# Optimization experiments

Measured on AMD Instinct MI355X. Metric: run time of the kernel, lower is better.

## Reference

```python
import jax, jax.numpy as jnp
import numpy as np

NUM_HEADS = 8
NUM_GROUPS = 32  # min(C//4, 32) for C=512
EPS = 1e-6       # flax GroupNorm default


def setup_inputs() -> dict:
    key = jax.random.key(0)
    ks = jax.random.split(key, 3)
    B, H, W, D, C = 2, 16, 16, 16, 512
    x = jax.random.normal(ks[0], (B, H, W, D, C), dtype=jnp.float32)
    w_qkv = jax.random.normal(ks[1], (C, 3 * C), dtype=jnp.float32) / np.sqrt(C)
    w_proj = jax.random.normal(ks[2], (C, C), dtype=jnp.float32) / np.sqrt(C)
    return {
        "x": x,
        "gn_scale": jnp.ones((C,), jnp.float32),
        "gn_bias": jnp.zeros((C,), jnp.float32),
        "w_qkv": w_qkv,
        "b_qkv": jnp.zeros((3 * C,), jnp.float32),
        "w_proj": w_proj,
        "b_proj": jnp.zeros((C,), jnp.float32),
    }


def group_norm(x, scale, bias):
    # x: [B, S, C]; normalize within each of NUM_GROUPS channel groups over (S, group-channels)
    B, S, C = x.shape
    xg = x.reshape(B, S, NUM_GROUPS, C // NUM_GROUPS)
    mean = jnp.mean(xg, axis=(1, 3), keepdims=True)
    var = jnp.var(xg, axis=(1, 3), keepdims=True)
    xn = (xg - mean) * jax.lax.rsqrt(var + EPS)
    return xn.reshape(B, S, C) * scale + bias


def reference(x, gn_scale, gn_bias, w_qkv, b_qkv, w_proj, b_proj):
    B, H, W, D, C = x.shape
    S = H * W * D
    hd = C // NUM_HEADS
    xf = x.reshape(B, S, C)
    q_in = group_norm(xf, gn_scale, gn_bias)
    # 1x1x1 conv == per-position dense
    qkv = q_in @ w_qkv + b_qkv                      # [B, S, 3C]
    qkv = qkv.reshape(B, S, NUM_HEADS, 3 * hd)
    q, k, v = jnp.split(qkv, 3, axis=-1)            # each [B, S, nh, hd]
    scale = 1.0 / jnp.sqrt(jnp.asarray(hd, x.dtype))
    logits = jnp.einsum('btnh,bfnh->bnft', k, q * scale)  # [B, nh, S, S]
    weights = jax.nn.softmax(logits, axis=-1)
    h = jnp.einsum('bnft,btnh->bfnh', weights, v)   # [B, S, nh, hd]
    h = h.reshape(B, S, C) @ w_proj + b_proj
    return h.reshape(x.shape) + x
```

## Files before the change

### kernel.cpp

```cpp
#include <hip/hip_runtime.h>

typedef __attribute__((ext_vector_type(8))) short short8;
typedef __attribute__((ext_vector_type(4))) float f32x4;
typedef __attribute__((ext_vector_type(16))) float f32x16;

#define S_LEN 4096
#define C_DIM 512
#define NH 8
#define HD 64
#define NG 32
#define GS 16
#define LOG2E 1.44269504088896340736f

__device__ __forceinline__ unsigned short f2bf(float f) {
  union { float f; unsigned int u; } v; v.f = f;
  unsigned int r = v.u + 0x7fffu + ((v.u >> 16) & 1u);
  return (unsigned short)(r >> 16);
}

__device__ __forceinline__ float fexp2(float x) {
  float r;
  asm("v_exp_f32 %0, %1" : "=v"(r) : "v"(x));
  return r;
}

__device__ __forceinline__ unsigned pk_bf16(float a, float b) {
  unsigned r;
  asm("v_cvt_pk_bf16_f32 %0, %1, %2" : "=v"(r) : "v"(a), "v"(b));
  return r;
}

__device__ __forceinline__ void pl_swap(unsigned& a, unsigned& b) {
  asm("v_permlane32_swap_b32 %0, %1" : "+v"(a), "+v"(b));
}

__device__ __forceinline__ void gload_lds16(const void* g, void* l) {
  __builtin_amdgcn_global_load_lds((const __attribute__((address_space(1))) void*)g,
                                   (__attribute__((address_space(3))) void*)l, 16, 0, 0);
}

__global__ __launch_bounds__(256) void prep_kernel(const float* __restrict__ x,
                                                   float* __restrict__ partials,
                                                   const float* __restrict__ w_qkv,
                                                   unsigned short* __restrict__ wqkvT,
                                                   const float* __restrict__ w_proj,
                                                   unsigned short* __restrict__ wprojT) {
  __shared__ float tile[32][33];
  __shared__ float r1[4], r2[4];
  int bid = blockIdx.x;
  if (bid < 256) {
    int bg = bid >> 2, chunk = bid & 3;
    int b = bg >> 5, g = bg & 31;
    const float* xp = x + (size_t)b * S_LEN * C_DIM + g * GS;
    float s1 = 0.f, s2 = 0.f;
    for (int i = threadIdx.x; i < 1024 * 4; i += 256) {
      int s = chunk * 1024 + (i >> 2), c4 = i & 3;
      float4 v = *(const float4*)&xp[(size_t)s * C_DIM + c4 * 4];
      s1 += v.x + v.y + v.z + v.w;
      s2 += v.x * v.x + v.y * v.y + v.z * v.z + v.w * v.w;
    }
    for (int off = 1; off < 64; off <<= 1) {
      s1 += __shfl_xor(s1, off);
      s2 += __shfl_xor(s2, off);
    }
    int w = threadIdx.x >> 6;
    if ((threadIdx.x & 63) == 0) { r1[w] = s1; r2[w] = s2; }
    __syncthreads();
    if (threadIdx.x == 0) {
      partials[bg * 8 + chunk * 2]     = r1[0] + r1[1] + r1[2] + r1[3];
      partials[bg * 8 + chunk * 2 + 1] = r2[0] + r2[1] + r2[2] + r2[3];
    }
    return;
  }
  const float* src; unsigned short* dst; int K, N, n0, k0;
  if (bid < 1024) {
    int t = bid - 256;  src = w_qkv;  dst = wqkvT;  K = 512; N = 1536;
    n0 = (t % 48) * 32; k0 = (t / 48) * 32;
  } else {
    int t = bid - 1024; src = w_proj; dst = wprojT; K = 512; N = 512;
    n0 = (t % 16) * 32; k0 = (t / 16) * 32;
  }
  int c = threadIdx.x & 31, r0 = threadIdx.x >> 5;
  for (int i = 0; i < 4; ++i) {
    int r = r0 + i * 8;
    tile[r][c] = src[(size_t)(k0 + r) * N + n0 + c];
  }
  __syncthreads();
  for (int i = 0; i < 4; ++i) {
    int r = r0 + i * 8;
    dst[(size_t)(n0 + r) * K + k0 + c] = f2bf(tile[c][r]);
  }
}

__global__ __launch_bounds__(256) void gn_apply_kernel(const float* __restrict__ x,
                                                       const float* __restrict__ partials,
                                                       const float* __restrict__ scale,
                                                       const float* __restrict__ bias,
                                                       unsigned short* __restrict__ out) {
  int idx = blockIdx.x * 256 + threadIdx.x;
  int e = idx * 4;
  int c = e & (C_DIM - 1);
  int bs = e >> 9;
  int b = bs >> 12;
  int grp = b * NG + (c >> 4);
  float s1 = partials[grp * 8] + partials[grp * 8 + 2] + partials[grp * 8 + 4] + partials[grp * 8 + 6];
  float s2 = partials[grp * 8 + 1] + partials[grp * 8 + 3] + partials[grp * 8 + 5] + partials[grp * 8 + 7];
  const float invN = 1.0f / (float)(S_LEN * GS);
  float mean = s1 * invN;
  float var = s2 * invN - mean * mean;
  float rstd = rsqrtf(var + 1e-6f);
  float4 v = *(const float4*)&x[e];
  ushort4 o;
  o.x = f2bf((v.x - mean) * rstd * scale[c]     + bias[c]);
  o.y = f2bf((v.y - mean) * rstd * scale[c + 1] + bias[c + 1]);
  o.z = f2bf((v.z - mean) * rstd * scale[c + 2] + bias[c + 2]);
  o.w = f2bf((v.w - mean) * rstd * scale[c + 3] + bias[c + 3]);
  *(ushort4*)&out[e] = o;
}

template <int MODE>
__global__ __launch_bounds__(256) void gemm_kernel(const unsigned short* __restrict__ A,
                                                   const unsigned short* __restrict__ Bt,
                                                   const float* __restrict__ bias,
                                                   unsigned short* __restrict__ qh,
                                                   unsigned short* __restrict__ kh,
                                                   unsigned short* __restrict__ vh,
                                                   const float* __restrict__ resid,
                                                   float* __restrict__ outf,
                                                   int K) {
  __shared__ unsigned short Alds[128][72];
  __shared__ unsigned short Blds[128][72];
  int tid = threadIdx.x, lane = tid & 63, w = tid >> 6;
  int li = lane & 15, g = lane >> 4;
  int wr = (w >> 1) * 64, wc = (w & 1) * 64;
  int m0 = blockIdx.y * 128, n0 = blockIdx.x * 128;
  f32x4 acc[4][4];
  for (int i = 0; i < 4; ++i)
    for (int j = 0; j < 4; ++j) acc[i][j] = (f32x4){0.f, 0.f, 0.f, 0.f};

  for (int k0 = 0; k0 < K; k0 += 64) {
    for (int i = 0; i < 4; ++i) {
      int ch = tid + i * 256;
      int r = ch >> 3, c8 = (ch & 7) * 8;
      *(int4*)&Alds[r][c8] = *(const int4*)&A[(size_t)(m0 + r) * K + k0 + c8];
      *(int4*)&Blds[r][c8] = *(const int4*)&Bt[(size_t)(n0 + r) * K + k0 + c8];
    }
    __syncthreads();
    for (int ks = 0; ks < 2; ++ks) {
      short8 af[4], bfm[4];
      for (int mi = 0; mi < 4; ++mi)
        af[mi] = *(const short8*)&Alds[wr + mi * 16 + li][ks * 32 + g * 8];
      for (int ni = 0; ni < 4; ++ni)
        bfm[ni] = *(const short8*)&Blds[wc + ni * 16 + li][ks * 32 + g * 8];
      for (int mi = 0; mi < 4; ++mi)
        for (int ni = 0; ni < 4; ++ni)
          acc[mi][ni] = __builtin_amdgcn_mfma_f32_16x16x32_bf16(af[mi], bfm[ni], acc[mi][ni], 0, 0, 0);
    }
    __syncthreads();
  }

  if (MODE == 0) {
    for (int ni = 0; ni < 4; ++ni) {
      int n = n0 + wc + ni * 16 + li;
      float bn = bias[n];
      int head = n / 192;
      int rem = n - head * 192;
      int part = rem >> 6;
      int h = rem & 63;
      unsigned short* dst = part == 0 ? qh : (part == 1 ? kh : vh);
      float mul = part == 0 ? 0.125f * LOG2E : 1.0f;
      for (int mi = 0; mi < 4; ++mi)
        for (int j = 0; j < 4; ++j) {
          int m = m0 + wr + mi * 16 + g * 4 + j;
          int b = m >> 12, s = m & 4095;
          float val = (acc[mi][ni][j] + bn) * mul;
          size_t idx;
          if (part == 2) idx = ((size_t)(b * NH + head) * HD + h) * S_LEN + s;
          else           idx = ((size_t)(b * NH + head) * S_LEN + s) * HD + h;
          dst[idx] = f2bf(val);
        }
    }
  } else {
    for (int ni = 0; ni < 4; ++ni) {
      int n = n0 + wc + ni * 16 + li;
      float bn = bias[n];
      for (int mi = 0; mi < 4; ++mi)
        for (int j = 0; j < 4; ++j) {
          int m = m0 + wr + mi * 16 + g * 4 + j;
          size_t off = (size_t)m * C_DIM + n;
          outf[off] = acc[mi][ni][j] + bn + resid[off];
        }
    }
  }
}

template <int SPLIT>
__global__ __launch_bounds__(256, 4) void attn_kernel(const unsigned short* __restrict__ qh,
                                                      const unsigned short* __restrict__ kh,
                                                      const unsigned short* __restrict__ vt,
                                                      unsigned short* __restrict__ ob,
                                                      float* __restrict__ part) {
  __shared__ unsigned char Kt[2][4096];
  __shared__ unsigned char Vt[2][4096];
  int bn = blockIdx.y;
  int half = SPLIT == 2 ? blockIdx.z : 0;
  int tid = threadIdx.x, lane = tid & 63, wv = tid >> 6;
  int r32 = lane & 31, hi = lane >> 5;
  int q0 = blockIdx.x * 128 + wv * 32;
  const int NT = S_LEN / 32 / SPLIT;
  const unsigned short* qp = qh + (size_t)bn * S_LEN * HD;
  const char* kp = (const char*)(kh + (size_t)bn * S_LEN * HD);
  const char* vp = (const char*)(vt + (size_t)bn * HD * S_LEN);

  int srow  = wv * 8 + (lane >> 3);
  int scolS = (lane & 7) * 16;
  int sc    = scolS ^ ((srow & 7) << 4);
  const char* kSrc = kp + (size_t)srow * 128 + sc + (size_t)half * (S_LEN / 2) * 128;
  int vh_ = srow + ((sc >> 6) << 5);
  const char* vSrc = vp + (size_t)vh_ * (S_LEN * 2) + (sc & 63) + (size_t)half * (S_LEN / 2) * 2;

  short8 qf[4];
#pragma unroll
  for (int ks = 0; ks < 4; ++ks)
    qf[ks] = *(const short8*)&qp[(size_t)(q0 + r32) * HD + ks * 16 + hi * 8];

  union { unsigned u[4]; short8 v; } ones;
#pragma unroll
  for (int i = 0; i < 4; ++i) ones.u[i] = 0x3F803F80u;

  f32x16 o0, o1, lacc;
#pragma unroll
  for (int i = 0; i < 16; ++i) { o0[i] = 0.f; o1[i] = 0.f; lacc[i] = 0.f; }

  int swzr = (r32 & 7) << 4;
  const unsigned char* Kr0 = &Kt[0][r32 * 128];
  const unsigned char* Vr0 = &Vt[0][r32 * 128];

  gload_lds16(kSrc, &Kt[0][wv * 1024]);
  gload_lds16(vSrc, &Vt[0][wv * 1024]);
  __syncthreads();

  for (int it = 0; it < NT; ++it) {
    int buf = it & 1;
    if (it < NT - 1) {
      size_t t0n = (size_t)(it + 1) * 32;
      gload_lds16(kSrc + t0n * 128, &Kt[buf ^ 1][wv * 1024]);
      gload_lds16(vSrc + t0n * 2,   &Vt[buf ^ 1][wv * 1024]);
    }

    const unsigned char* Kr = Kr0 + buf * 4096;
    const unsigned char* Vr = Vr0 + buf * 4096;
    short8 kf[4], vf[4];
#pragma unroll
    for (int ks = 0; ks < 4; ++ks)
      kf[ks] = *(const short8*)&Kr[(ks * 32 + hi * 16) ^ swzr];
#pragma unroll
    for (int kk = 0; kk < 2; ++kk)
#pragma unroll
      for (int hf = 0; hf < 2; ++hf)
        vf[kk * 2 + hf] = *(const short8*)&Vr[(hf * 64 + kk * 32 + hi * 16) ^ swzr];

    f32x16 s;
#pragma unroll
    for (int i = 0; i < 16; ++i) s[i] = 0.f;
#pragma unroll
    for (int ks = 0; ks < 4; ++ks)
      s = __builtin_amdgcn_mfma_f32_32x32x16_bf16(kf[ks], qf[ks], s, 0, 0, 0);

#pragma unroll
    for (int i = 0; i < 16; ++i) s[i] = fexp2(s[i]);

    unsigned pkv[8];
#pragma unroll
    for (int g2 = 0; g2 < 8; ++g2) pkv[g2] = pk_bf16(s[2 * g2], s[2 * g2 + 1]);
    pl_swap(pkv[0], pkv[2]); pl_swap(pkv[1], pkv[3]);
    pl_swap(pkv[4], pkv[6]); pl_swap(pkv[5], pkv[7]);
    union { unsigned u[4]; short8 v; } F0, F1;
    F0.u[0] = pkv[0]; F0.u[1] = pkv[1]; F0.u[2] = pkv[2]; F0.u[3] = pkv[3];
    F1.u[0] = pkv[4]; F1.u[1] = pkv[5]; F1.u[2] = pkv[6]; F1.u[3] = pkv[7];

    o0 = __builtin_amdgcn_mfma_f32_32x32x16_bf16(vf[0], F0.v, o0, 0, 0, 0);
    o1 = __builtin_amdgcn_mfma_f32_32x32x16_bf16(vf[1], F0.v, o1, 0, 0, 0);
    lacc = __builtin_amdgcn_mfma_f32_32x32x16_bf16(ones.v, F0.v, lacc, 0, 0, 0);
    o0 = __builtin_amdgcn_mfma_f32_32x32x16_bf16(vf[2], F1.v, o0, 0, 0, 0);
    o1 = __builtin_amdgcn_mfma_f32_32x32x16_bf16(vf[3], F1.v, o1, 0, 0, 0);
    lacc = __builtin_amdgcn_mfma_f32_32x32x16_bf16(ones.v, F1.v, lacc, 0, 0, 0);

    __syncthreads();
  }

  if (SPLIT == 1) {
    float inv = 1.0f / lacc[0];
    int b = bn >> 3, n = bn & 7;
    size_t base = ((size_t)(b * S_LEN + q0 + r32)) * C_DIM + n * HD;
#pragma unroll
    for (int r = 0; r < 16; ++r) {
      int hrow = (r & 3) + 8 * (r >> 2) + 4 * hi;
      ob[base + hrow]      = f2bf(o0[r] * inv);
      ob[base + 32 + hrow] = f2bf(o1[r] * inv);
    }
  } else {
    float* pp = part + (((size_t)(bn * 2 + half) * S_LEN) + q0 + r32) * 68;
#pragma unroll
    for (int r = 0; r < 16; ++r) {
      int hrow = (r & 3) + 8 * (r >> 2) + 4 * hi;
      pp[hrow]      = o0[r];
      pp[32 + hrow] = o1[r];
    }
    if (!hi) pp[64] = lacc[0];
  }
}

__global__ __launch_bounds__(256) void attn_combine_kernel(const float* __restrict__ part,
                                                           unsigned short* __restrict__ ob) {
  int idx = blockIdx.x * 256 + threadIdx.x;
  int h0 = (idx & 7) * 8;
  int q  = (idx >> 3) & (S_LEN - 1);
  int bn = idx >> 15;
  const float* pA = part + (((size_t)(bn * 2 + 0) * S_LEN) + q) * 68;
  const float* pB = part + (((size_t)(bn * 2 + 1) * S_LEN) + q) * 68;
  float inv = 1.0f / (pA[64] + pB[64]);
  float4 a0 = *(const float4*)&pA[h0], a1 = *(const float4*)&pA[h0 + 4];
  float4 b0 = *(const float4*)&pB[h0], b1 = *(const float4*)&pB[h0 + 4];
  union { unsigned short us[8]; short8 v; } R;
  R.us[0] = f2bf((a0.x + b0.x) * inv); R.us[1] = f2bf((a0.y + b0.y) * inv);
  R.us[2] = f2bf((a0.z + b0.z) * inv); R.us[3] = f2bf((a0.w + b0.w) * inv);
  R.us[4] = f2bf((a1.x + b1.x) * inv); R.us[5] = f2bf((a1.y + b1.y) * inv);
  R.us[6] = f2bf((a1.z + b1.z) * inv); R.us[7] = f2bf((a1.w + b1.w) * inv);
  int b = bn >> 3, n = bn & 7;
  *(short8*)&ob[((size_t)(b * S_LEN + q)) * C_DIM + n * HD + h0] = R.v;
}

extern "C" void kernel_launch(void* const* d_in, const int* in_sizes, int n_in,
                              void* d_out, int out_size, void* d_ws, size_t ws_size,
                              hipStream_t stream) {
  const float* x        = (const float*)d_in[0];
  const float* gn_scale = (const float*)d_in[1];
  const float* gn_bias  = (const float*)d_in[2];
  const float* w_qkv    = (const float*)d_in[3];
  const float* b_qkv    = (const float*)d_in[4];
  const float* w_proj   = (const float*)d_in[5];
  const float* b_proj   = (const float*)d_in[6];
  float* out = (float*)d_out;

  char* ws = (char*)d_ws;
  unsigned short* q_in   = (unsigned short*)(ws);
  unsigned short* wqkvT  = (unsigned short*)(ws + 8388608);
  unsigned short* wprojT = (unsigned short*)(ws + 9961472);
  unsigned short* qhb    = (unsigned short*)(ws + 10485760);
  unsigned short* khb    = (unsigned short*)(ws + 18874368);
  unsigned short* vtb    = (unsigned short*)(ws + 27262976);
  unsigned short* ahb    = (unsigned short*)(ws + 35651584);
  float* partials        = (float*)(ws + 44040192);
  float* opart           = (float*)(ws + 44042240);
  const size_t WS_NEED_SPLIT = 44042240ull + (size_t)16 * 2 * S_LEN * 68 * 4;

  prep_kernel<<<1280, 256, 0, stream>>>(x, partials, w_qkv, wqkvT, w_proj, wprojT);
  gn_apply_kernel<<<4096, 256, 0, stream>>>(x, partials, gn_scale, gn_bias, q_in);
  gemm_kernel<0><<<dim3(12, 64), 256, 0, stream>>>(q_in, wqkvT, b_qkv, qhb, khb, vtb, nullptr, nullptr, 512);
  if (ws_size >= WS_NEED_SPLIT) {
    attn_kernel<2><<<dim3(32, 16, 2), 256, 0, stream>>>(qhb, khb, vtb, ahb, opart);
    attn_combine_kernel<<<2048, 256, 0, stream>>>(opart, ahb);
  } else {
    attn_kernel<1><<<dim3(32, 16, 1), 256, 0, stream>>>(qhb, khb, vtb, ahb, nullptr);
  }
  gemm_kernel<1><<<dim3(4, 64), 256, 0, stream>>>(ahb, wprojT, b_proj, nullptr, nullptr, nullptr, x, out, 512);
}
```

Before: 162.3 us.

## Triple-buffer attention K/V tiles and store split partials in bf16

The attention loop now uses three LDS buffers for K and V, prefetching two tiles ahead. Each iteration waits with an explicit vmcnt(2) wait plus a raw barrier instead of a full __syncthreads, so global loads overlap more with the MFMA work. The split-K partial outputs are stored as packed bf16 with a float row sum, which halves partial-buffer traffic in both the attention and combine kernels. The first QK MFMA also starts from a zero register instead of a zeroed accumulator. In exchange, LDS use grows, which can reduce occupancy, and the partials lose precision before the combine step.

```diff
diff --git a/kernel.cpp b/kernel.cpp
--- a/kernel.cpp
+++ b/kernel.cpp
@@ -199,9 +199,9 @@
                                                       const unsigned short* __restrict__ kh,
                                                       const unsigned short* __restrict__ vt,
                                                       unsigned short* __restrict__ ob,
-                                                      float* __restrict__ part) {
-  __shared__ unsigned char Kt[2][4096];
-  __shared__ unsigned char Vt[2][4096];
+                                                      unsigned short* __restrict__ part) {
+  __shared__ unsigned char Kt[3 * 4096];
+  __shared__ unsigned char Vt[3 * 4096];
   int bn = blockIdx.y;
   int half = SPLIT == 2 ? blockIdx.z : 0;
   int tid = threadIdx.x, lane = tid & 63, wv = tid >> 6;
@@ -228,28 +228,31 @@
 #pragma unroll
   for (int i = 0; i < 4; ++i) ones.u[i] = 0x3F803F80u;
 
-  f32x16 o0, o1, lacc;
-#pragma unroll
-  for (int i = 0; i < 16; ++i) { o0[i] = 0.f; o1[i] = 0.f; lacc[i] = 0.f; }
+  f32x16 o0, o1, lacc, z16;
+#pragma unroll
+  for (int i = 0; i < 16; ++i) { o0[i] = 0.f; o1[i] = 0.f; lacc[i] = 0.f; z16[i] = 0.f; }
 
   int swzr = (r32 & 7) << 4;
-  const unsigned char* Kr0 = &Kt[0][r32 * 128];
-  const unsigned char* Vr0 = &Vt[0][r32 * 128];
-
-  gload_lds16(kSrc, &Kt[0][wv * 1024]);
-  gload_lds16(vSrc, &Vt[0][wv * 1024]);
-  __syncthreads();
-
+  int sBase = wv * 1024;
+
+  gload_lds16(kSrc, &Kt[sBase]);
+  gload_lds16(vSrc, &Vt[sBase]);
+  gload_lds16(kSrc + 32 * 128, &Kt[4096 + sBase]);
+  gload_lds16(vSrc + 32 * 2,   &Vt[4096 + sBase]);
+  asm volatile("s_waitcnt vmcnt(2)" ::: "memory");
+  __builtin_amdgcn_s_barrier();
+
+  int curO = 0, nxtO = 4096, nnO = 8192;
   for (int it = 0; it < NT; ++it) {
-    int buf = it & 1;
-    if (it < NT - 1) {
-      size_t t0n = (size_t)(it + 1) * 32;
-      gload_lds16(kSrc + t0n * 128, &Kt[buf ^ 1][wv * 1024]);
-      gload_lds16(vSrc + t0n * 2,   &Vt[buf ^ 1][wv * 1024]);
-    }
-
-    const unsigned char* Kr = Kr0 + buf * 4096;
-    const unsigned char* Vr = Vr0 + buf * 4096;
+    bool more = (it + 2 < NT);
+    if (more) {
+      size_t t0n = (size_t)(it + 2) * 32;
+      gload_lds16(kSrc + t0n * 128, &Kt[nnO + sBase]);
+      gload_lds16(vSrc + t0n * 2,   &Vt[nnO + sBase]);
+    }
+
+    const unsigned char* Kr = &Kt[curO + r32 * 128];
+    const unsigned char* Vr = &Vt[curO + r32 * 128];
     short8 kf[4], vf[4];
 #pragma unroll
     for (int ks = 0; ks < 4; ++ks)
@@ -260,11 +263,9 @@
       for (int hf = 0; hf < 2; ++hf)
         vf[kk * 2 + hf] = *(const short8*)&Vr[(hf * 64 + kk * 32 + hi * 16) ^ swzr];
 
-    f32x16 s;
-#pragma unroll
-    for (int i = 0; i < 16; ++i) s[i] = 0.f;
-#pragma unroll
-    for (int ks = 0; ks < 4; ++ks)
+    f32x16 s = __builtin_amdgcn_mfma_f32_32x32x16_bf16(kf[0], qf[0], z16, 0, 0, 0);
+#pragma unroll
+    for (int ks = 1; ks < 4; ++ks)
       s = __builtin_amdgcn_mfma_f32_32x32x16_bf16(kf[ks], qf[ks], s, 0, 0, 0);
 
 #pragma unroll
@@ -286,7 +287,10 @@
     o1 = __builtin_amdgcn_mfma_f32_32x32x16_bf16(vf[3], F1.v, o1, 0, 0, 0);
     lacc = __builtin_amdgcn_mfma_f32_32x32x16_bf16(ones.v, F1.v, lacc, 0, 0, 0);
 
-    __syncthreads();
+    if (more) asm volatile("s_waitcnt vmcnt(2)" ::: "memory");
+    else      asm volatile("s_waitcnt vmcnt(0)" ::: "memory");
+    __builtin_amdgcn_s_barrier();
+    int t = curO; curO = nxtO; nxtO = nnO; nnO = t;
   }
 
   if (SPLIT == 1) {
@@ -300,35 +304,39 @@
       ob[base + 32 + hrow] = f2bf(o1[r] * inv);
     }
   } else {
-    float* pp = part + (((size_t)(bn * 2 + half) * S_LEN) + q0 + r32) * 68;
-#pragma unroll
-    for (int r = 0; r < 16; ++r) {
+    unsigned short* pp = part + (((size_t)(bn * 2 + half) * S_LEN) + q0 + r32) * 72;
+#pragma unroll
+    for (int i = 0; i < 8; ++i) {
+      int r = 2 * i;
       int hrow = (r & 3) + 8 * (r >> 2) + 4 * hi;
-      pp[hrow]      = o0[r];
-      pp[32 + hrow] = o1[r];
-    }
-    if (!hi) pp[64] = lacc[0];
-  }
-}
-
-__global__ __launch_bounds__(256) void attn_combine_kernel(const float* __restrict__ part,
+      *(unsigned*)&pp[hrow]      = pk_bf16(o0[r], o0[r + 1]);
+      *(unsigned*)&pp[32 + hrow] = pk_bf16(o1[r], o1[r + 1]);
+    }
+    if (!hi) *(float*)&pp[64] = lacc[0];
+  }
+}
+
+__global__ __launch_bounds__(256) void attn_combine_kernel(const unsigned short* __restrict__ part,
                                                            unsigned short* __restrict__ ob) {
   int idx = blockIdx.x * 256 + threadIdx.x;
   int h0 = (idx & 7) * 8;
   int q  = (idx >> 3) & (S_LEN - 1);
   int bn = idx >> 15;
-  const float* pA = part + (((size_t)(bn * 2 + 0) * S_LEN) + q) * 68;
-  const float* pB = part + (((size_t)(bn * 2 + 1) * S_LEN) + q) * 68;
-  float inv = 1.0f / (pA[64] + pB[64]);
-  float4 a0 = *(const float4*)&pA[h0], a1 = *(const float4*)&pA[h0 + 4];
-  float4 b0 = *(const float4*)&pB[h0], b1 = *(const float4*)&pB[h0 + 4];
+  const unsigned short* pA = part + (((size_t)(bn * 2 + 0) * S_LEN) + q) * 72;
+  const unsigned short* pB = part + (((size_t)(bn * 2 + 1) * S_LEN) + q) * 72;
+  float inv = 1.0f / (*(const float*)&pA[64] + *(const float*)&pB[64]);
+  short8 a = *(const short8*)&pA[h0];
+  short8 b = *(const short8*)&pB[h0];
   union { unsigned short us[8]; short8 v; } R;
-  R.us[0] = f2bf((a0.x + b0.x) * inv); R.us[1] = f2bf((a0.y + b0.y) * inv);
-  R.us[2] = f2bf((a0.z + b0.z) * inv); R.us[3] = f2bf((a0.w + b0.w) * inv);
-  R.us[4] = f2bf((a1.x + b1.x) * inv); R.us[5] = f2bf((a1.y + b1.y) * inv);
-  R.us[6] = f2bf((a1.z + b1.z) * inv); R.us[7] = f2bf((a1.w + b1.w) * inv);
-  int b = bn >> 3, n = bn & 7;
-  *(short8*)&ob[((size_t)(b * S_LEN + q)) * C_DIM + n * HD + h0] = R.v;
+#pragma unroll
+  for (int j = 0; j < 8; ++j) {
+    union { unsigned u; float f; } fa, fb;
+    fa.u = (unsigned)(unsigned short)a[j] << 16;
+    fb.u = (unsigned)(unsigned short)b[j] << 16;
+    R.us[j] = f2bf((fa.f + fb.f) * inv);
+  }
+  int b_ = bn >> 3, n = bn & 7;
+  *(short8*)&ob[((size_t)(b_ * S_LEN + q)) * C_DIM + n * HD + h0] = R.v;
 }
 
 extern "C" void kernel_launch(void* const* d_in, const int* in_sizes, int n_in,
@@ -352,8 +360,8 @@
   unsigned short* vtb    = (unsigned short*)(ws + 27262976);
   unsigned short* ahb    = (unsigned short*)(ws + 35651584);
   float* partials        = (float*)(ws + 44040192);
-  float* opart           = (float*)(ws + 44042240);
-  const size_t WS_NEED_SPLIT = 44042240ull + (size_t)16 * 2 * S_LEN * 68 * 4;
+  unsigned short* opart  = (unsigned short*)(ws + 44042240);
+  const size_t WS_NEED_SPLIT = 44042240ull + (size_t)16 * 2 * S_LEN * 72 * 2;
 
   prep_kernel<<<1280, 256, 0, stream>>>(x, partials, w_qkv, wqkvT, w_proj, wprojT);
   gn_apply_kernel<<<4096, 256, 0, stream>>>(x, partials, gn_scale, gn_bias, q_in);
```

Measured after the change: 156.8 us. -3.4%, faster.
